# Kernel optimization log

Measured on AMD Instinct MI355X. Metric: run time of the kernel, lower is better.

The kernel has to match this reference:

```python
import jax, jax.numpy as jnp
import numpy as np

KSIZE = 7
STRIDE = 4
SCALE = 10.0


def _same_pad(n, k, s):
    # torch 'same' padding used in extract_image_patches (asymmetric)
    out = -(-n // s)
    pad = max(0, (out - 1) * s + k - n)
    top = pad // 2
    return (top, pad - top)


def _conv1x1(x, W, b):
    # x: [C,H,W], W: [O,C], b: [O]
    return jnp.einsum('oc,chw->ohw', W, x) + b[:, None, None]


def _unfold(x, k, s, pad_h, pad_w):
    # x: [C,H,W] -> patches [Lh*Lw, C*k*k] in (C, kh, kw) order (torch Unfold order)
    C = x.shape[0]
    xp = jnp.pad(x, ((0, 0), pad_h, pad_w))
    Hp, Wp = xp.shape[1], xp.shape[2]
    Lh = (Hp - k) // s + 1
    Lw = (Wp - k) // s + 1
    ih = (jnp.arange(Lh) * s)[:, None] + jnp.arange(k)  # [Lh,k]
    iw = (jnp.arange(Lw) * s)[:, None] + jnp.arange(k)  # [Lw,k]
    p = xp[:, ih][:, :, :, iw]                # [C,Lh,k,Lw,k]
    p = p.transpose(1, 3, 0, 2, 4).reshape(Lh * Lw, C * k * k)
    return p, Lh, Lw


def _fold(p, Lh, Lw, C, k, s, H, W, pad):
    # p: [Lh*Lw, C*k*k] -> overlap-summed image [C,H,W] (torch F.fold, symmetric pad)
    P = p.reshape(Lh, Lw, C, k, k).transpose(2, 0, 1, 3, 4)  # [C,Lh,Lw,k,k]
    Hp, Wp = H + 2 * pad, W + 2 * pad
    ih = (jnp.arange(Lh) * s)[:, None] + jnp.arange(k)  # [Lh,k]
    iw = (jnp.arange(Lw) * s)[:, None] + jnp.arange(k)  # [Lw,k]
    IH = ih[:, None, :, None]  # broadcast -> [Lh,Lw,k,k]
    IW = iw[None, :, None, :]
    canvas = jnp.zeros((C, Hp, Wp), p.dtype).at[:, IH, IW].add(P)
    return canvas[:, pad:pad + H, pad:pad + W]


def _salsa_one(x, Wg, bg, Wt, bt, Wp, bp, Ww, bw):
    # x: [C,H,W]
    C, H, W = x.shape
    ic = Wg.shape[0]
    k, s = KSIZE, STRIDE
    ph = _same_pad(H, k, s)
    pw = _same_pad(W, k, s)
    q, Lh, Lw = _unfold(_conv1x1(x, Wg, bg), k, s, ph, pw)   # g   -> queries [L, ic*k*k]
    kk, _, _ = _unfold(_conv1x1(x, Wp, bp), k, s, ph, pw)    # phi -> keys
    v, _, _ = _unfold(_conv1x1(x, Wt, bt), k, s, ph, pw)     # theta -> values
    att = jax.nn.softmax((q @ kk.T) * SCALE, axis=1)         # [L1,L2]
    out = att @ v                                            # [L1, ic*k*k]
    fp = (k - 1) // 2  # paddings[0] from stride-1 same_padding in the original (=3)
    zi = _fold(out, Lh, Lw, ic, k, s, H, W, fp)
    ones_p, mLh, mLw = _unfold(jnp.ones((ic, H, W), x.dtype), k, s, (fp, fp), (fp, fp))
    mask = _fold(ones_p, mLh, mLw, ic, k, s, H, W, fp)
    zi = zi / mask
    return x + _conv1x1(zi, Ww, bw)


def setup_inputs() -> dict:
    key = jax.random.key(0)
    B, C, H, W, IC = 4, 64, 256, 256, 16
    ks = jax.random.split(key, 9)
    sC = 1.0 / np.sqrt(C)
    sI = 1.0 / np.sqrt(IC)
    return {
        'b': jax.random.normal(ks[0], (B, C, H, W), jnp.float32),
        'Wg': jax.random.normal(ks[1], (IC, C), jnp.float32) * sC,
        'bg': jax.random.normal(ks[2], (IC,), jnp.float32) * 0.01,
        'Wt': jax.random.normal(ks[3], (IC, C), jnp.float32) * sC,
        'bt': jax.random.normal(ks[4], (IC,), jnp.float32) * 0.01,
        'Wp': jax.random.normal(ks[5], (IC, C), jnp.float32) * sC,
        'bp': jax.random.normal(ks[6], (IC,), jnp.float32) * 0.01,
        'Ww': jax.random.normal(ks[7], (C, IC), jnp.float32) * sI,
        'bw': jax.random.normal(ks[8], (C,), jnp.float32) * 0.01,
    }


def reference(b, Wg, bg, Wt, bt, Wp, bp, Ww, bw):
    f = jax.vmap(_salsa_one, in_axes=(0, None, None, None, None, None, None, None, None))
    return f(b, Wg, bg, Wt, bt, Wp, bp, Ww, bw)
```

## Files before the change

### kernel.cpp

```cpp
#include <hip/hip_runtime.h>

#define CIN 64
#define ICN 16
#define HH 256
#define WID 256
#define HW (HH*WID)
#define LL 4096
#define KD 784
#define KDP 800
#define KQ 832
#define NVT 896
#define NB 4

typedef __attribute__((ext_vector_type(8))) short short8;
typedef __attribute__((ext_vector_type(4))) float f32x4;
typedef __attribute__((ext_vector_type(4))) int i32x4;

__device__ __forceinline__ unsigned short f2bf(float x){
  union { float f; unsigned u; } v; v.f = x;
  unsigned r = v.u + 0x7FFF + ((v.u >> 16) & 1);
  return (unsigned short)(r >> 16);
}

__global__ __launch_bounds__(256) void conv1x1_3(
    const float* __restrict__ x,
    const float* __restrict__ Wg, const float* __restrict__ bg,
    const float* __restrict__ Wp, const float* __restrict__ bp,
    const float* __restrict__ Wt, const float* __restrict__ bt,
    float* __restrict__ G, float* __restrict__ P, float* __restrict__ T) {
  __shared__ float wg[ICN*CIN], wp[ICN*CIN], wt[ICN*CIN];
  int t = threadIdx.x;
  for (int i = t; i < ICN*CIN; i += 256) { wg[i]=Wg[i]; wp[i]=Wp[i]; wt[i]=Wt[i]; }
  __syncthreads();
  int p = blockIdx.x*256 + t;
  float aG[ICN], aP[ICN], aT[ICN];
#pragma unroll
  for (int o=0;o<ICN;o++){ aG[o]=bg[o]; aP[o]=bp[o]; aT[o]=bt[o]; }
  for (int c=0;c<CIN;c++){
    float xv = x[c*HW + p];
#pragma unroll
    for (int o=0;o<ICN;o++){
      aG[o] = fmaf(wg[o*CIN+c], xv, aG[o]);
      aP[o] = fmaf(wp[o*CIN+c], xv, aP[o]);
      aT[o] = fmaf(wt[o*CIN+c], xv, aT[o]);
    }
  }
#pragma unroll
  for (int o=0;o<ICN;o++){ G[o*HW+p]=aG[o]; P[o*HW+p]=aP[o]; T[o*HW+p]=aT[o]; }
}

__global__ __launch_bounds__(256) void unfold_qk_q(
    const float* __restrict__ G, const float* __restrict__ P,
    char* __restrict__ Q0, char* __restrict__ Q1,
    char* __restrict__ K0, char* __restrict__ K1,
    float* __restrict__ sQ, float* __restrict__ sK){
  __shared__ float gb[KQ], pb[KQ];
  __shared__ float redg[256], redp[256];
  int row = blockIdx.x;
  int iy = row >> 6, ix = row & 63;
  int t = threadIdx.x;
  float gmax = 0.f, pmax = 0.f;
  for (int col = t; col < KQ; col += 256){
    float g = 0.f, p = 0.f;
    if (col < KD){
      int c = col / 49; int r = col - c*49; int dy = r / 7; int dx = r - dy*7;
      int y = (iy<<2) + dy - 1, x = (ix<<2) + dx - 1;
      if ((unsigned)y < HH && (unsigned)x < WID){
        int a = c*HW + (y<<8) + x;
        g = G[a]; p = P[a];
      }
    }
    gb[col] = g; pb[col] = p;
    gmax = fmaxf(gmax, fabsf(g)); pmax = fmaxf(pmax, fabsf(p));
  }
  redg[t]=gmax; redp[t]=pmax; __syncthreads();
  for (int s2=128;s2>0;s2>>=1){
    if (t<s2){ redg[t]=fmaxf(redg[t],redg[t+s2]); redp[t]=fmaxf(redp[t],redp[t+s2]); }
    __syncthreads();
  }
  float mg = redg[0], mp = redp[0];
  float rsg = mg > 0.f ? mg*(1.f/127.f) : 1.f;
  float rsp = mp > 0.f ? mp*(1.f/127.f) : 1.f;
  if (t==0){ sQ[row]=rsg; sK[row]=rsp; }
  float ig = 1.f/rsg, ip = 1.f/rsp;
  if (t < KQ/4){
    char q0[4],q1[4],k0[4],k1[4];
#pragma unroll
    for (int u=0;u<4;u++){
      float xg = gb[t*4+u]*ig;
      float a0 = rintf(xg);
      int ia1 = (int)rintf((xg - a0)*256.f);
      ia1 = ia1>127?127:(ia1<-127?-127:ia1);
      q0[u] = (char)(int)a0; q1[u] = (char)ia1;
      float xp = pb[t*4+u]*ip;
      float b0 = rintf(xp);
      int ib1 = (int)rintf((xp - b0)*256.f);
      ib1 = ib1>127?127:(ib1<-127?-127:ib1);
      k0[u] = (char)(int)b0; k1[u] = (char)ib1;
    }
    size_t o = (size_t)row*KQ + t*4;
    *(char4*)(Q0+o) = make_char4(q0[0],q0[1],q0[2],q0[3]);
    *(char4*)(Q1+o) = make_char4(q1[0],q1[1],q1[2],q1[3]);
    *(char4*)(K0+o) = make_char4(k0[0],k0[1],k0[2],k0[3]);
    *(char4*)(K1+o) = make_char4(k1[0],k1[1],k1[2],k1[3]);
  }
}

__global__ __launch_bounds__(256) void unfold_vt(
    const float* __restrict__ T, unsigned short* __restrict__ Vt){
  int idx = blockIdx.x*256 + threadIdx.x;
  int col = idx >> 12, row = idx & 4095;
  float t = 0.f;
  if (col < KD){
    int c = col / 49; int r = col - c*49; int dy = r / 7; int dx = r - dy*7;
    int iy = row >> 6, ix = row & 63;
    int y = (iy<<2) + dy - 1, x = (ix<<2) + dx - 1;
    if ((unsigned)y < HH && (unsigned)x < WID) t = T[c*HW + (y<<8) + x];
  }
  Vt[idx] = f2bf(t);
}

__global__ __launch_bounds__(256) void gemm_qk_i8(
    const char* __restrict__ Q0, const char* __restrict__ Q1,
    const char* __restrict__ K0, const char* __restrict__ K1,
    const float* __restrict__ sQ, const float* __restrict__ sK,
    float* __restrict__ ATT){
  __shared__ alignas(16) char lds[4][128*64];
  const int tid = threadIdx.x;
  const int lane = tid & 63, w = tid >> 6;
  const int wr = w >> 1, wc = w & 1;
  const int row0 = blockIdx.y*128, col0 = blockIdx.x*128;

  const char* base;
  { const char* s0[4] = {
      Q0 + (size_t)row0*KQ, Q1 + (size_t)row0*KQ,
      K0 + (size_t)col0*KQ, K1 + (size_t)col0*KQ };
    base = s0[w]; }

  const int r_lo = lane >> 2, slot = lane & 3;
  int goff[8];
#pragma unroll
  for (int j=0;j<8;j++){
    int r = j*16 + r_lo;
    goff[j] = r*KQ + ((slot ^ ((r>>1)&3))<<4);
  }

  const int lrow = lane & 15, g = lane >> 4;
  int offA[4], offB[4];
#pragma unroll
  for (int i=0;i<4;i++){
    int rA = wr*64 + i*16 + lrow;
    offA[i] = rA*64 + ((g ^ ((rA>>1)&3))<<4);
    int rB = wc*64 + i*16 + lrow;
    offB[i] = rB*64 + ((g ^ ((rB>>1)&3))<<4);
  }

  i32x4 accH[4][4] = {};
  i32x4 accC[4][4] = {};

  for (int kb = 0; kb < KQ; kb += 64){
#pragma unroll
    for (int j=0;j<8;j++)
      __builtin_amdgcn_global_load_lds(
        (const __attribute__((address_space(1))) void*)(base + goff[j] + kb),
        (__attribute__((address_space(3))) void*)(&lds[w][j*1024]), 16, 0, 0);
    __syncthreads();
    i32x4 a0[4], a1[4], b0[4], b1[4];
#pragma unroll
    for (int i=0;i<4;i++){
      a0[i] = *(const i32x4*)&lds[0][offA[i]];
      a1[i] = *(const i32x4*)&lds[1][offA[i]];
      b0[i] = *(const i32x4*)&lds[2][offB[i]];
      b1[i] = *(const i32x4*)&lds[3][offB[i]];
    }
#pragma unroll
    for (int i=0;i<4;i++)
#pragma unroll
      for (int j=0;j<4;j++){
        accH[i][j] = __builtin_amdgcn_mfma_i32_16x16x64_i8(a0[i], b0[j], accH[i][j], 0,0,0);
        accC[i][j] = __builtin_amdgcn_mfma_i32_16x16x64_i8(a0[i], b1[j], accC[i][j], 0,0,0);
        accC[i][j] = __builtin_amdgcn_mfma_i32_16x16x64_i8(a1[i], b0[j], accC[i][j], 0,0,0);
      }
    __syncthreads();
  }

#pragma unroll
  for (int j=0;j<4;j++){
    int col = col0 + wc*64 + j*16 + lrow;
    float cs = sK[col]*10.f;
#pragma unroll
    for (int i=0;i<4;i++){
#pragma unroll
      for (int r=0;r<4;r++){
        int row = row0 + wr*64 + i*16 + g*4 + r;
        float rs = sQ[row];
        ATT[(size_t)row*LL + col] =
          rs*cs*((float)accH[i][j][r] + (float)accC[i][j][r]*0.00390625f);
      }
    }
  }
}

__global__ __launch_bounds__(256) void softmax_rows(
    const float* __restrict__ ATT, unsigned short* __restrict__ Pb){
  __shared__ float red[256];
  int t = threadIdx.x;
  const float* r = ATT + (size_t)blockIdx.x * LL;
  unsigned short* po = Pb + (size_t)blockIdx.x * LL;
  float v[16];
  float mx = -3.4e38f;
#pragma unroll
  for (int i=0;i<16;i++){ v[i] = r[t + (i<<8)]; mx = fmaxf(mx, v[i]); }
  red[t] = mx; __syncthreads();
  for (int s2=128;s2>0;s2>>=1){ if (t<s2) red[t]=fmaxf(red[t],red[t+s2]); __syncthreads(); }
  mx = red[0]; __syncthreads();
  float sum = 0.f;
#pragma unroll
  for (int i=0;i<16;i++){ v[i] = __expf(v[i]-mx); sum += v[i]; }
  red[t]=sum; __syncthreads();
  for (int s2=128;s2>0;s2>>=1){ if (t<s2) red[t]+=red[t+s2]; __syncthreads(); }
  float inv = 1.0f / red[0];
#pragma unroll
  for (int i=0;i<16;i++) po[t+(i<<8)] = f2bf(v[i]*inv);
}

__global__ __launch_bounds__(256) void gemm_pv_mfma(
    const unsigned short* __restrict__ Pb, const unsigned short* __restrict__ Vt,
    float* __restrict__ OUT){
  __shared__ alignas(16) short ldsA[128*32];
  __shared__ alignas(16) short ldsB[128*32];
  const int tid = threadIdx.x;
  const int lane = tid & 63, w = tid >> 6;
  const int wr = w >> 1, wc = w & 1;
  const int row0 = blockIdx.y*128, col0 = blockIdx.x*128;

  const unsigned short* baseA = Pb + (size_t)row0*LL;
  const unsigned short* baseB = Vt + (size_t)col0*LL;
  const int r_lo = lane >> 2, slot = lane & 3;
  int goff0, goff1;
  { int r = w*16 + r_lo;       goff0 = r*LL + ((slot ^ ((r>>1)&3))<<3); }
  { int r = (4+w)*16 + r_lo;   goff1 = r*LL + ((slot ^ ((r>>1)&3))<<3); }

  const int lrow = lane & 15, g = lane >> 4;
  int offA[4], offB[4];
#pragma unroll
  for (int i=0;i<4;i++){
    int rA = wr*64 + i*16 + lrow;
    offA[i] = rA*32 + ((g ^ ((rA>>1)&3))<<3);
    int rB = wc*64 + i*16 + lrow;
    offB[i] = rB*32 + ((g ^ ((rB>>1)&3))<<3);
  }

  f32x4 acc[4][4] = {};

  for (int kb = 0; kb < LL; kb += 32){
    __builtin_amdgcn_global_load_lds(
      (const __attribute__((address_space(1))) void*)(baseA + goff0 + kb),
      (__attribute__((address_space(3))) void*)(&ldsA[w*512]), 16, 0, 0);
    __builtin_amdgcn_global_load_lds(
      (const __attribute__((address_space(1))) void*)(baseA + goff1 + kb),
      (__attribute__((address_space(3))) void*)(&ldsA[(4+w)*512]), 16, 0, 0);
    __builtin_amdgcn_global_load_lds(
      (const __attribute__((address_space(1))) void*)(baseB + goff0 + kb),
      (__attribute__((address_space(3))) void*)(&ldsB[w*512]), 16, 0, 0);
    __builtin_amdgcn_global_load_lds(
      (const __attribute__((address_space(1))) void*)(baseB + goff1 + kb),
      (__attribute__((address_space(3))) void*)(&ldsB[(4+w)*512]), 16, 0, 0);
    __syncthreads();
    short8 a[4], b[4];
#pragma unroll
    for (int i=0;i<4;i++){
      a[i] = *(const short8*)&ldsA[offA[i]];
      b[i] = *(const short8*)&ldsB[offB[i]];
    }
#pragma unroll
    for (int i=0;i<4;i++)
#pragma unroll
      for (int j=0;j<4;j++)
        acc[i][j] = __builtin_amdgcn_mfma_f32_16x16x32_bf16(a[i], b[j], acc[i][j], 0,0,0);
    __syncthreads();
  }

#pragma unroll
  for (int i=0;i<4;i++)
#pragma unroll
    for (int j=0;j<4;j++){
      int col = col0 + wc*64 + j*16 + lrow;
      if (col < KD){
#pragma unroll
        for (int r=0;r<4;r++)
          OUT[(size_t)(row0 + wr*64 + i*16 + g*4 + r)*KDP + col] = acc[i][j][r];
      }
    }
}

__global__ __launch_bounds__(256) void fold_final(
    const float* __restrict__ OUT, const float* __restrict__ xin,
    const float* __restrict__ Ww, const float* __restrict__ bw,
    float* __restrict__ out){
  __shared__ float wsh[CIN*ICN];
  __shared__ float bsh[CIN];
  int t = threadIdx.x;
  for (int i=t;i<CIN*ICN;i+=256) wsh[i]=Ww[i];
  if (t<CIN) bsh[t]=bw[t];
  __syncthreads();
  int p = blockIdx.x*256 + t;
  int y = p >> 8, x = p & 255;
  int yc = y + 3, xc = x + 3;
  int i0 = (yc-3) >> 2; int i1 = yc >> 2; if (i1 > 63) i1 = 63;
  int j0 = (xc-3) >> 2; int j1 = xc >> 2; if (j1 > 63) j1 = 63;
  float zi[ICN] = {};
  for (int i = i0; i <= i1; i++){
    int dy = yc - (i<<2);
    for (int j = j0; j <= j1; j++){
      int dx = xc - (j<<2);
      const float* bp = &OUT[(size_t)((i<<6)+j)*KDP + dy*7 + dx];
#pragma unroll
      for (int c=0;c<ICN;c++) zi[c] += bp[c*49];
    }
  }
  float inv = 1.0f / (float)((i1-i0+1)*(j1-j0+1));
#pragma unroll
  for (int c=0;c<ICN;c++) zi[c] *= inv;
#pragma unroll
  for (int co=0;co<CIN;co++){
    float acc = xin[co*HW + p] + bsh[co];
    const float4* w4 = (const float4*)&wsh[co*ICN];
#pragma unroll
    for (int c4=0;c4<4;c4++){
      float4 wv = w4[c4];
      acc = fmaf(wv.x, zi[c4*4+0], acc);
      acc = fmaf(wv.y, zi[c4*4+1], acc);
      acc = fmaf(wv.z, zi[c4*4+2], acc);
      acc = fmaf(wv.w, zi[c4*4+3], acc);
    }
    out[co*HW + p] = acc;
  }
}

extern "C" void kernel_launch(void* const* d_in, const int* in_sizes, int n_in,
                              void* d_out, int out_size, void* d_ws, size_t ws_size,
                              hipStream_t stream) {
  const float* xb = (const float*)d_in[0];
  const float* Wg = (const float*)d_in[1];
  const float* bg = (const float*)d_in[2];
  const float* Wt = (const float*)d_in[3];
  const float* bt = (const float*)d_in[4];
  const float* Wp = (const float*)d_in[5];
  const float* bp = (const float*)d_in[6];
  const float* Ww = (const float*)d_in[7];
  const float* bw = (const float*)d_in[8];
  float* out = (float*)d_out;

  char* ws = (char*)d_ws;
  float*          G   = (float*)(ws + 0);
  float*          Pc  = (float*)(ws + 4194304);
  float*          T   = (float*)(ws + 8388608);
  char*           Q0  = (char*)(ws + 12582912);
  char*           Q1  = (char*)(ws + 15990784);
  char*           K0  = (char*)(ws + 19398656);
  char*           K1  = (char*)(ws + 22806528);
  float*          sQ  = (float*)(ws + 26214400);
  float*          sK  = (float*)(ws + 26230784);
  float*          ATT = (float*)(ws + 33554432);
  unsigned short* Vt  = (unsigned short*)(ws + 100663296);
  unsigned short* Pb  = (unsigned short*)(ws + 0);
  float*          OUTm= (float*)(ws + 33554432);

  for (int b = 0; b < NB; b++){
    const float* x = xb + (size_t)b*CIN*HW;
    conv1x1_3<<<HW/256, 256, 0, stream>>>(x, Wg,bg, Wp,bp, Wt,bt, G,Pc,T);
    unfold_qk_q<<<LL, 256, 0, stream>>>(G, Pc, Q0, Q1, K0, K1, sQ, sK);
    unfold_vt<<<NVT*LL/256, 256, 0, stream>>>(T, Vt);
    gemm_qk_i8<<<dim3(LL/128, LL/128), 256, 0, stream>>>(Q0, Q1, K0, K1, sQ, sK, ATT);
    softmax_rows<<<LL, 256, 0, stream>>>(ATT, Pb);
    gemm_pv_mfma<<<dim3(NVT/128, LL/128), 256, 0, stream>>>(Pb, Vt, OUTm);
    fold_final<<<HW/256, 256, 0, stream>>>(OUTm, x, Ww, bw, out + (size_t)b*CIN*HW);
  }
}
```

Measured before the change: 1.189 ms.

## Split-K the PV GEMM with a reduction kernel and vectorize softmax I/O

The PV GEMM grid was only 7x32=224 blocks, which underfills the GPU, so it now splits the K dimension into four chunks along blockIdx.z. Each chunk writes a partial result, and a new pv_reduce kernel sums the four partials. The softmax kernel also switches to float4 loads and ushort4 stores to cut memory instructions. The split adds writes and reads of partial buffers (about 4x13MB) plus an extra kernel launch. It also needs the workspace after offset 33.5MB to hold four partials, and the space it overwrites is the ATT region that has already been consumed.

```diff
diff --git a/kernel.cpp b/kernel.cpp
--- a/kernel.cpp
+++ b/kernel.cpp
@@ -11,6 +11,8 @@
 #define KQ 832
 #define NVT 896
 #define NB 4
+#define SPLITK 4
+#define KCH (LL/SPLITK)
 
 typedef __attribute__((ext_vector_type(8))) short short8;
 typedef __attribute__((ext_vector_type(4))) float f32x4;
@@ -205,34 +207,48 @@
     const float* __restrict__ ATT, unsigned short* __restrict__ Pb){
   __shared__ float red[256];
   int t = threadIdx.x;
-  const float* r = ATT + (size_t)blockIdx.x * LL;
-  unsigned short* po = Pb + (size_t)blockIdx.x * LL;
-  float v[16];
+  const float4* r4 = (const float4*)(ATT + (size_t)blockIdx.x * LL);
+  ushort4* po = (ushort4*)(Pb + (size_t)blockIdx.x * LL);
+  float4 v[4];
   float mx = -3.4e38f;
 #pragma unroll
-  for (int i=0;i<16;i++){ v[i] = r[t + (i<<8)]; mx = fmaxf(mx, v[i]); }
+  for (int i=0;i<4;i++){
+    v[i] = r4[t + (i<<8)];
+    mx = fmaxf(mx, fmaxf(fmaxf(v[i].x, v[i].y), fmaxf(v[i].z, v[i].w)));
+  }
   red[t] = mx; __syncthreads();
   for (int s2=128;s2>0;s2>>=1){ if (t<s2) red[t]=fmaxf(red[t],red[t+s2]); __syncthreads(); }
   mx = red[0]; __syncthreads();
   float sum = 0.f;
 #pragma unroll
-  for (int i=0;i<16;i++){ v[i] = __expf(v[i]-mx); sum += v[i]; }
+  for (int i=0;i<4;i++){
+    v[i].x = __expf(v[i].x-mx); v[i].y = __expf(v[i].y-mx);
+    v[i].z = __expf(v[i].z-mx); v[i].w = __expf(v[i].w-mx);
+    sum += v[i].x + v[i].y + v[i].z + v[i].w;
+  }
   red[t]=sum; __syncthreads();
   for (int s2=128;s2>0;s2>>=1){ if (t<s2) red[t]+=red[t+s2]; __syncthreads(); }
   float inv = 1.0f / red[0];
 #pragma unroll
-  for (int i=0;i<16;i++) po[t+(i<<8)] = f2bf(v[i]*inv);
+  for (int i=0;i<4;i++){
+    ushort4 o;
+    o.x = f2bf(v[i].x*inv); o.y = f2bf(v[i].y*inv);
+    o.z = f2bf(v[i].z*inv); o.w = f2bf(v[i].w*inv);
+    po[t + (i<<8)] = o;
+  }
 }
 
 __global__ __launch_bounds__(256) void gemm_pv_mfma(
     const unsigned short* __restrict__ Pb, const unsigned short* __restrict__ Vt,
-    float* __restrict__ OUT){
+    float* __restrict__ OUTP){
   __shared__ alignas(16) short ldsA[128*32];
   __shared__ alignas(16) short ldsB[128*32];
   const int tid = threadIdx.x;
   const int lane = tid & 63, w = tid >> 6;
   const int wr = w >> 1, wc = w & 1;
   const int row0 = blockIdx.y*128, col0 = blockIdx.x*128;
+  const int z = blockIdx.z;
+  float* OUT = OUTP + (size_t)z * LL * KDP;
 
   const unsigned short* baseA = Pb + (size_t)row0*LL;
   const unsigned short* baseB = Vt + (size_t)col0*LL;
@@ -253,7 +269,8 @@
 
   f32x4 acc[4][4] = {};
 
-  for (int kb = 0; kb < LL; kb += 32){
+  const int kend = (z+1)*KCH;
+  for (int kb = z*KCH; kb < kend; kb += 32){
     __builtin_amdgcn_global_load_lds(
       (const __attribute__((address_space(1))) void*)(baseA + goff0 + kb),
       (__attribute__((address_space(3))) void*)(&ldsA[w*512]), 16, 0, 0);
@@ -292,6 +309,19 @@
           OUT[(size_t)(row0 + wr*64 + i*16 + g*4 + r)*KDP + col] = acc[i][j][r];
       }
     }
+}
+
+__global__ __launch_bounds__(256) void pv_reduce(float* __restrict__ P){
+  const size_t PL = (size_t)LL*KDP/4;
+  size_t idx = (size_t)blockIdx.x*256 + threadIdx.x;
+  if (idx >= PL) return;
+  float4* p = (float4*)P;
+  float4 a = p[idx], b = p[idx+PL], c = p[idx+2*PL], d = p[idx+3*PL];
+  a.x += b.x + c.x + d.x;
+  a.y += b.y + c.y + d.y;
+  a.z += b.z + c.z + d.z;
+  a.w += b.w + c.w + d.w;
+  p[idx] = a;
 }
 
 __global__ __launch_bounds__(256) void fold_final(
@@ -365,7 +395,7 @@
   float*          ATT = (float*)(ws + 33554432);
   unsigned short* Vt  = (unsigned short*)(ws + 100663296);
   unsigned short* Pb  = (unsigned short*)(ws + 0);
-  float*          OUTm= (float*)(ws + 33554432);
+  float*          OUTP= (float*)(ws + 33554432);
 
   for (int b = 0; b < NB; b++){
     const float* x = xb + (size_t)b*CIN*HW;
@@ -374,7 +404,8 @@
     unfold_vt<<<NVT*LL/256, 256, 0, stream>>>(T, Vt);
     gemm_qk_i8<<<dim3(LL/128, LL/128), 256, 0, stream>>>(Q0, Q1, K0, K1, sQ, sK, ATT);
     softmax_rows<<<LL, 256, 0, stream>>>(ATT, Pb);
-    gemm_pv_mfma<<<dim3(NVT/128, LL/128), 256, 0, stream>>>(Pb, Vt, OUTm);
-    fold_final<<<HW/256, 256, 0, stream>>>(OUTm, x, Ww, bw, out + (size_t)b*CIN*HW);
-  }
-}
+    gemm_pv_mfma<<<dim3(NVT/128, LL/128, SPLITK), 256, 0, stream>>>(Pb, Vt, OUTP);
+    pv_reduce<<<(LL*KDP/4 + 255)/256, 256, 0, stream>>>(OUTP);
+    fold_final<<<HW/256, 256, 0, stream>>>(OUTP, x, Ww, bw, out + (size_t)b*CIN*HW);
+  }
+}
```

Result: no change. 1.191 ms (+0.1%).
